# Performance work log

Hardware: AMD Instinct MI355X
Metric: run time of the kernel (lower is better)

Reference implementation:

```python
import jax, jax.numpy as jnp
import numpy as np

K = 20
EPS = 1e-6


def _vnt_linear(x, W):
    # VNT linear: rows normalized to sum to 1 (translation-equivariant channel mix)
    Wn = W / W.sum(axis=1, keepdims=True)
    return jnp.einsum('oi,bi...->bo...', Wn, x)


def _vn_lrelu(p, d):
    # Vector-neuron LeakyReLU with negative_slope=0: project p off -d half-space
    dot = jnp.sum(p * d, axis=2, keepdims=True)   # axis 2 is the 3-vector axis
    dns = jnp.sum(d * d, axis=2, keepdims=True)
    return jnp.where(dot >= 0, p, p - (dot / (dns + EPS)) * d)


def _vnt_lin_lrelu(x, W, D):
    p = _vnt_linear(x, W)
    d = jnp.einsum('oi,bi...->bo...', D, x)
    return _vn_lrelu(p, d)


def _graph_feature_cross(pts, k):
    # pts: [B, N, 3] -> edge features [B, 3(ch), 3(vec), N, k]
    B = pts.shape[0]
    xx = jnp.sum(pts * pts, axis=-1)                       # [B, N]
    inner = jnp.einsum('bnd,bmd->bnm', pts, pts)           # [B, N, N]
    pairwise = 2.0 * inner - xx[:, :, None] - xx[:, None, :]  # -||xi-xj||^2
    _, idx = jax.lax.top_k(pairwise, k)                    # [B, N, k]
    b_idx = jnp.arange(B)[:, None, None]
    nbrs = pts[b_idx, idx]                                 # [B, N, k, 3]
    ctr = jnp.broadcast_to(pts[:, :, None, :], nbrs.shape)
    cross = jnp.cross(nbrs, ctr)
    feat = jnp.stack([nbrs - ctr, ctr, cross], axis=3)     # [B, N, k, 3ch, 3vec]
    return jnp.transpose(feat, (0, 3, 4, 1, 2))            # [B, 3, 3, N, k]


def setup_inputs() -> dict:
    key = jax.random.key(0)
    ks = jax.random.split(key, 9)
    B, N, hidden = 8, 2048, 128

    def w(k_, o, i):  # positive weights -> stable row-sum normalization
        return jax.random.uniform(k_, (o, i), jnp.float32, 0.5 / i, 1.5 / i)

    def d(k_, o, i):
        return jax.random.normal(k_, (o, i), jnp.float32) / np.sqrt(i)

    return {
        'pc': jax.random.normal(ks[0], (B, N, 3), jnp.float32),
        'W_pos': w(ks[1], 64, 3), 'D_pos': d(ks[2], 64, 3),
        'W1': w(ks[3], hidden, 64), 'D1': d(ks[4], hidden, 64),
        'W2': w(ks[5], hidden, 2 * hidden), 'D2': d(ks[6], hidden, 2 * hidden),
        'W3': w(ks[7], hidden, 2 * hidden), 'D3': d(ks[8], hidden, 2 * hidden),
    }


def reference(pc, W_pos, D_pos, W1, D1, W2, D2, W3, D3):
    feat = _graph_feature_cross(pc, K)               # [B, 3, 3, N, k]
    net = _vnt_lin_lrelu(feat, W_pos, D_pos)         # [B, 64, 3, N, k]
    net = net.mean(axis=-1)                          # pool over k -> [B, 64, 3, N]
    net = _vnt_lin_lrelu(net, W1, D1)                # [B, 128, 3, N]
    pooled = jnp.broadcast_to(net.mean(axis=-1, keepdims=True), net.shape)
    net = jnp.concatenate([net, pooled], axis=1)     # [B, 256, 3, N]
    net = _vnt_lin_lrelu(net, W2, D2)                # [B, 128, 3, N]
    pooled = jnp.broadcast_to(net.mean(axis=-1, keepdims=True), net.shape)
    net = jnp.concatenate([net, pooled], axis=1)     # [B, 256, 3, N]
    net = _vnt_lin_lrelu(net, W3, D3)                # [B, 128, 3, N]
    c = net.mean(axis=-1)                            # pool over N -> [B, 128, 3]
    return c.reshape(pc.shape[0], -1)                # [B, 384]
```

## Files before the change

kernel.cpp:

```cpp
#include <hip/hip_runtime.h>
#include <hip/hip_bf16.h>
#include <math.h>

constexpr int B = 8;
constexpr int N = 2048;
constexpr int KNN = 20;
constexpr int H = 128;
constexpr int P = 3 * N;
constexpr int QPW = 8;

constexpr int OWT2   = 8448;
constexpr int OWT3   = 41216;
constexpr int OPS1   = 73984;
constexpr int OPS2   = 98560;
constexpr int OOUTS  = 123136;
constexpr int OWB1   = 160000;
constexpr int OWB2   = 176384;
constexpr int OWB3   = 209152;
constexpr int OXP0   = 569600;
constexpr int OXP2   = 569600;
constexpr int OXP1   = 6861056;

constexpr int ZERO_BASE = OPS1;
constexpr int ZERO_CNT  = 73728;

typedef __attribute__((ext_vector_type(8))) short bf16x8;
typedef __attribute__((ext_vector_type(4))) float f32x4;

__device__ __forceinline__ unsigned short f2bf(float x) {
  __hip_bfloat16 h = __float2bfloat16(x);
  return *(unsigned short*)&h;
}
__device__ __forceinline__ float bf2f(unsigned short u) {
  __hip_bfloat16 h;
  *(unsigned short*)&h = u;
  return __bfloat162float(h);
}
__device__ __forceinline__ unsigned int packhl(float x) {
  unsigned short hi = f2bf(x);
  float lo = x - bf2f(hi);
  unsigned short ls = f2bf(lo);
  return (unsigned)hi | ((unsigned)ls << 16);
}

__device__ __forceinline__ void wave_sort_key(unsigned long long& k, int lane) {
#pragma unroll
  for (int kk = 2; kk <= 64; kk <<= 1) {
#pragma unroll
    for (int j = kk >> 1; j > 0; j >>= 1) {
      unsigned long long pk =
          (unsigned long long)__shfl_xor((long long)k, j);
      bool iam_lower   = (lane & j) == 0;
      bool dir_desc    = (lane & kk) == 0;
      bool p_better    = pk > k;
      bool want_better = (dir_desc == iam_lower);
      k = (p_better == want_better) ? pk : k;
    }
  }
}

__global__ __launch_bounds__(512, 8) void knn_edge_kernel(
    const float* __restrict__ pc, const float* __restrict__ Wpos,
    const float* __restrict__ Dp,
    const float* __restrict__ W1, const float* __restrict__ D1,
    const float* __restrict__ W2, const float* __restrict__ D2,
    const float* __restrict__ W3, const float* __restrict__ D3,
    float* __restrict__ ws) {
  __shared__ float4 spt[N];
  __shared__ __align__(16) unsigned char sphase[QPW][640];
  int tid = threadIdx.x;
  int b = blockIdx.y;
  int bid = blockIdx.y * gridDim.x + blockIdx.x;
  int wv = tid >> 6, lane = tid & 63;
  unsigned short* Xp0 = (unsigned short*)(ws + OXP0);
  unsigned short* sbufw = (unsigned short*)sphase[wv];
  float4* erw = (float4*)sphase[wv];

  int o = lane;
  float w0 = Wpos[o * 3 + 0], w1 = Wpos[o * 3 + 1], w2 = Wpos[o * 3 + 2];
  float e0 = Dp[o * 3 + 0], e1 = Dp[o * 3 + 1], e2 = Dp[o * 3 + 2];

  {
    int zi = bid * 512 + tid;
    if (zi < ZERO_CNT) ws[ZERO_BASE + zi] = 0.f;
  }
  if (bid < 96) {
    int rr = bid * 8 + wv;
    const float* src;
    float* tdst = nullptr;
    unsigned int* pdst;
    int C, Cpack;
    bool norm;
    if (rr < 128)      { src = W1 + rr * 64;            C = 64;  Cpack = 64;  norm = true;
                         pdst = (unsigned int*)(ws + OWB1) + rr * 16; }
    else if (rr < 256) { int m = rr - 128; src = D1 + m * 64;  C = 64;  Cpack = 64;  norm = false;
                         pdst = (unsigned int*)(ws + OWB1) + (m + 128) * 16; }
    else if (rr < 384) { int m = rr - 256; src = W2 + m * 256; C = 256; Cpack = 128; norm = true;
                         pdst = (unsigned int*)(ws + OWB2) + m * 16; tdst = ws + OWT2 + m; }
    else if (rr < 512) { int m = rr - 384; src = D2 + m * 256; C = 256; Cpack = 128; norm = false;
                         pdst = (unsigned int*)(ws + OWB2) + (m + 128) * 16; tdst = ws + OWT2 + 128 + m; }
    else if (rr < 640) { int m = rr - 512; src = W3 + m * 256; C = 256; Cpack = 128; norm = true;
                         pdst = (unsigned int*)(ws + OWB3) + m * 16; tdst = ws + OWT3 + m; }
    else               { int m = rr - 640; src = D3 + m * 256; C = 256; Cpack = 128; norm = false;
                         pdst = (unsigned int*)(ws + OWB3) + (m + 128) * 16; tdst = ws + OWT3 + 128 + m; }
    float s = 1.f;
    if (norm) {
      float a = 0.f;
      for (int i = lane; i < C; i += 64) a += src[i];
#pragma unroll
      for (int off = 32; off > 0; off >>= 1) a += __shfl_xor(a, off);
      s = a;
    }
    for (int i = lane; i < C; i += 64) {
      float val = src[i] / s;
      if (i < Cpack) pdst[(i >> 4) * 4096 + (i & 15)] = packhl(val);
      if (tdst && i >= 128) tdst[(i - 128) * 256] = val;
    }
  }

  const float* pcb = pc + (size_t)b * N * 3;
  for (int i = tid; i < N; i += 512) {
    float x = pcb[i * 3 + 0], y = pcb[i * 3 + 1], z = pcb[i * 3 + 2];
    float xx = __fadd_rn(__fadd_rn(__fmul_rn(x, x), __fmul_rn(y, y)), __fmul_rn(z, z));
    spt[i] = make_float4(2.f * x, 2.f * y, 2.f * z, xx);
  }
  __syncthreads();
  int q = blockIdx.x * QPW + wv;
  float4 qp = spt[q];
  float qx = 0.5f * qp.x, qy = 0.5f * qp.y, qz = 0.5f * qp.z, qxx = qp.w;

  float dv[32];
  float lmax = -INFINITY;
#pragma unroll
  for (int i = 0; i < 32; ++i) {
    float4 m = spt[i * 64 + lane];
    float A = __fadd_rn(__fadd_rn(__fmul_rn(m.x, qx), __fmul_rn(m.y, qy)),
                        __fmul_rn(m.z, qz));
    float d = __fsub_rn(__fsub_rn(A, qxx), m.w);
    dv[i] = d;
    lmax = fmaxf(lmax, d);
  }

  float sv = lmax;
#pragma unroll
  for (int k = 2; k <= 64; k <<= 1) {
#pragma unroll
    for (int j = k >> 1; j > 0; j >>= 1) {
      float pv = __shfl_xor(sv, j);
      bool keep_max = ((lane & k) == 0) == ((lane & j) == 0);
      sv = keep_max ? fmaxf(sv, pv) : fminf(sv, pv);
    }
  }
  float tval = __shfl(sv, 19);

  unsigned msk = 0u;
#pragma unroll
  for (int i = 0; i < 32; ++i) msk |= (dv[i] >= tval) ? (1u << i) : 0u;
  int cnt = __popc(msk);
  int scan = cnt;
#pragma unroll
  for (int off = 1; off < 64; off <<= 1) {
    int t = __shfl_up(scan, off);
    scan += (lane >= off) ? t : 0;
  }
  int S = __shfl(scan, 63);
  int pos = scan - cnt;
  unsigned mm = msk;
  while (mm) {
    int i = __ffs(mm) - 1;
    mm &= mm - 1;
    if (pos < 192) sbufw[pos] = (unsigned short)(i * 64 + lane);
    ++pos;
  }

  auto distOf = [&](int m) -> float {
    float4 mp = spt[m];
    float A = __fadd_rn(__fadd_rn(__fmul_rn(mp.x, qx), __fmul_rn(mp.y, qy)),
                        __fmul_rn(mp.z, qz));
    return __fsub_rn(__fsub_rn(A, qxx), mp.w);
  };
  auto mkkey = [&](int m) -> unsigned long long {
    float d = distOf(m);
    unsigned u = __float_as_uint(d);
    u ^= (u >> 31) ? 0xFFFFFFFFu : 0x80000000u;
    return ((unsigned long long)u << 32) | (unsigned)(~m);
  };

  unsigned long long key = 0ULL;
  if (S <= 64) {
    if (lane < S) key = mkkey(sbufw[lane]);
    wave_sort_key(key, lane);
  } else if (S <= 192) {
    int p2 = 0;
    while (p2 < S) {
      if (lane >= KNN) {
        int t = p2 + lane - KNN;
        key = (t < S) ? mkkey(sbufw[t]) : 0ULL;
      }
      wave_sort_key(key, lane);
      p2 += 64 - KNN;
    }
  } else {
    int p2 = 0;
    while (p2 < N) {
      if (lane >= KNN) {
        int t = p2 + lane - KNN;
        key = (t < N) ? mkkey(t) : 0ULL;
      }
      wave_sort_key(key, lane);
      p2 += 64 - KNN;
    }
  }
  int cm = ~((unsigned)key);

  if (lane < KNN) {
    float4 t = spt[cm];
    float nx = 0.5f * t.x, ny = 0.5f * t.y, nz = 0.5f * t.z;
    float ex = nx - qx, ey = ny - qy, ez = nz - qz;
    float rx = ny * qz - nz * qy;
    float ry = nz * qx - nx * qz;
    float rz = nx * qy - ny * qx;
    erw[2 * lane + 0] = make_float4(ex, ey, ez, 0.f);
    erw[2 * lane + 1] = make_float4(rx, ry, rz, 0.f);
  }

  {
    float s = (w0 + w2) + w1;
    w0 = w0 / s; w1 = w1 / s; w2 = w2 / s;
  }
  float cx = qx, cy = qy, cz = qz;
  float pcx = w1 * cx, pcy = w1 * cy, pcz = w1 * cz;
  float dcx = e1 * cx, dcy = e1 * cy, dcz = e1 * cz;
  float ax = 0.f, ay = 0.f, az = 0.f;
#pragma unroll 4
  for (int k = 0; k < KNN; ++k) {
    float4 e4 = erw[2 * k + 0];
    float4 r4 = erw[2 * k + 1];
    float ex = e4.x, ey = e4.y, ez = e4.z;
    float rx = r4.x, ry = r4.y, rz = r4.z;
    float px = fmaf(w0, ex, fmaf(w2, rx, pcx));
    float py = fmaf(w0, ey, fmaf(w2, ry, pcy));
    float pz = fmaf(w0, ez, fmaf(w2, rz, pcz));
    float dx = fmaf(e0, ex, fmaf(e2, rx, dcx));
    float dy = fmaf(e0, ey, fmaf(e2, ry, dcy));
    float dz = fmaf(e0, ez, fmaf(e2, rz, dcz));
    float dot = fmaf(px, dx, fmaf(py, dy, pz * dz));
    float dns = fmaf(dx, dx, fmaf(dy, dy, dz * dz)) + 1e-6f;
    float r0 = __builtin_amdgcn_rcpf(dns);
    r0 = r0 * fmaf(-dns, r0, 2.0f);
    float f = (dot < 0.f) ? dot * r0 : 0.f;
    ax = fmaf(-f, dx, px) + ax;
    ay = fmaf(-f, dy, py) + ay;
    az = fmaf(-f, dz, pz) + az;
  }
  int pbase = ((q >> 4) * 48) + (q & 15);
  unsigned short* dst = Xp0 + ((size_t)b * P + pbase) * 128 + 2 * o;
  *(unsigned int*)(dst)              = packhl(ax * (1.f / 20.f));
  *(unsigned int*)(dst + 16 * 128)   = packhl(ay * (1.f / 20.f));
  *(unsigned int*)(dst + 32 * 128)   = packhl(az * (1.f / 20.f));
}

__global__ __launch_bounds__(256) void out_merge_kernel(
    const float* __restrict__ outs, float* __restrict__ out) {
  int idx = blockIdx.x * 256 + threadIdx.x;
  if (idx >= B * 384) return;
  float s = 0.f;
#pragma unroll
  for (int k = 0; k < 8; ++k) s += outs[k * 3072 + idx];
  out[idx] = s * (1.f / 2048.f);
}

template <int K2, bool HASPOOL, bool LAST>
__global__ __launch_bounds__(256, 4) void gemm_vnt_kernel(
    const unsigned short* __restrict__ Xp, const unsigned short* __restrict__ Wb,
    const float* __restrict__ ps, const float* __restrict__ Wt,
    unsigned short* __restrict__ Xq, float* __restrict__ pool,
    float* __restrict__ outs) {
  constexpr int KS = K2 / 32;
  constexpr int LDR = K2 + 8;
  constexpr int LDO = 132;
  __shared__ __align__(16) char smem[48 * LDO * 4];
  unsigned short* xt = (unsigned short*)smem;
  float* ot = (float*)smem;
  __shared__ float sb[768];
  __shared__ float spool[384];
  int tid = threadIdx.x;
  int bid = blockIdx.x;
  int b = bid >> 7;
  int nt = bid & 127;
  int p0 = nt * 48;

  int w = tid >> 6, lane = tid & 63;
  int q = lane >> 4, cl = lane & 15;

  for (int ch = tid; ch < 48 * (K2 / 8); ch += 256) {
    int rp = ch / (K2 / 8), cc = ch % (K2 / 8);
    *(uint4*)(xt + rp * LDR + cc * 8) =
        *(const uint4*)(Xp + ((size_t)b * P + p0 + rp) * K2 + cc * 8);
  }
  if (HASPOOL) {
    for (int i = tid; i < 384; i += 256) {
      float x = 0.f;
#pragma unroll
      for (int k = 0; k < 8; ++k) x += ps[k * 3072 + b * 384 + i];
      spool[i] = x * (1.f / 2048.f);
    }
  }

  bf16x8 acur[2][2], anxt[2][2];
#pragma unroll
  for (int t = 0; t < 2; ++t)
#pragma unroll
    for (int pd = 0; pd < 2; ++pd)
      acur[t][pd] = *(const bf16x8*)(Wb +
          (size_t)(32 * w + 16 * t + 128 * pd + cl) * 32 + q * 8);

  __syncthreads();
  if (HASPOOL) {
    float s0 = 0.f, s1 = 0.f, s2 = 0.f;
#pragma unroll 16
    for (int c = 0; c < 128; ++c) {
      float x = Wt[c * 256 + tid];
      s0 = fmaf(x, spool[c * 3 + 0], s0);
      s1 = fmaf(x, spool[c * 3 + 1], s1);
      s2 = fmaf(x, spool[c * 3 + 2], s2);
    }
    sb[tid * 3 + 0] = s0;
    sb[tid * 3 + 1] = s1;
    sb[tid * 3 + 2] = s2;
    __syncthreads();
  }

  f32x4 acc[2][2][3] = {};

#pragma unroll
  for (int ks = 0; ks < KS; ++ks) {
    if (ks + 1 < KS) {
#pragma unroll
      for (int t = 0; t < 2; ++t)
#pragma unroll
        for (int pd = 0; pd < 2; ++pd)
          anxt[t][pd] = *(const bf16x8*)(Wb +
              (size_t)(32 * w + 16 * t + 128 * pd + cl) * 32 + q * 8 +
              (ks + 1) * 8192);
    }
    bf16x8 bb[3];
#pragma unroll
    for (int v = 0; v < 3; ++v)
      bb[v] = *(const bf16x8*)(xt + (v * 16 + cl) * LDR + ks * 32 + q * 8);
#pragma unroll
    for (int t = 0; t < 2; ++t)
#pragma unroll
      for (int pd = 0; pd < 2; ++pd)
#pragma unroll
        for (int v = 0; v < 3; ++v)
          acc[t][pd][v] = __builtin_amdgcn_mfma_f32_16x16x32_bf16(
              acur[t][pd], bb[v], acc[t][pd][v], 0, 0, 0);
#pragma unroll
    for (int t = 0; t < 2; ++t)
#pragma unroll
      for (int pd = 0; pd < 2; ++pd)
        acur[t][pd] = anxt[t][pd];
  }
  __syncthreads();

#pragma unroll
  for (int t = 0; t < 2; ++t) {
    float res[3][4];
#pragma unroll
    for (int r = 0; r < 4; ++r) {
      int o = 32 * w + 16 * t + 4 * q + r;
      float pv[3], dvv[3];
#pragma unroll
      for (int v = 0; v < 3; ++v) {
        pv[v] = acc[t][0][v][r] + (HASPOOL ? sb[o * 3 + v] : 0.f);
        dvv[v] = acc[t][1][v][r] + (HASPOOL ? sb[(128 + o) * 3 + v] : 0.f);
      }
      float dot = fmaf(pv[0], dvv[0], fmaf(pv[1], dvv[1], pv[2] * dvv[2]));
      float dns = fmaf(dvv[0], dvv[0], fmaf(dvv[1], dvv[1], dvv[2] * dvv[2]));
      float f = (dot < 0.f) ? dot / (dns + 1e-6f) : 0.f;
#pragma unroll
      for (int v = 0; v < 3; ++v) res[v][r] = pv[v] - f * dvv[v];
    }
    int o0 = 32 * w + 16 * t + 4 * q;
#pragma unroll
    for (int v = 0; v < 3; ++v) {
      f32x4 rv = {res[v][0], res[v][1], res[v][2], res[v][3]};
      *(f32x4*)(ot + (v * 16 + cl) * LDO + o0) = rv;
    }
  }
  __syncthreads();

  int shadow = (nt & 7) * 3072;
  for (int s = tid; s < 384; s += 256) {
    int o = s / 3, v = s % 3;
    float a2 = 0.f;
#pragma unroll
    for (int c = 0; c < 16; ++c) a2 += ot[(v * 16 + c) * LDO + o];
    if (LAST) atomicAdd(outs + shadow + b * 384 + s, a2);
    else      atomicAdd(pool + shadow + b * 384 + s, a2);
  }

  if (!LAST) {
    for (int s = tid; s < 1536; s += 256) {
      int pix = s >> 5, c4 = s & 31;
      const float* src = ot + pix * LDO + c4 * 4;
      uint4 vv;
      vv.x = packhl(src[0]);
      vv.y = packhl(src[1]);
      vv.z = packhl(src[2]);
      vv.w = packhl(src[3]);
      *(uint4*)(Xq + ((size_t)b * P + p0 + pix) * 256 + c4 * 8) = vv;
    }
  }
}

extern "C" void kernel_launch(void* const* d_in, const int* in_sizes, int n_in,
                              void* d_out, int out_size, void* d_ws, size_t ws_size,
                              hipStream_t stream) {
  (void)in_sizes; (void)n_in; (void)out_size; (void)ws_size;
  const float* pc   = (const float*)d_in[0];
  const float* Wpos = (const float*)d_in[1];
  const float* Dpos = (const float*)d_in[2];
  const float* W1   = (const float*)d_in[3];
  const float* D1   = (const float*)d_in[4];
  const float* W2   = (const float*)d_in[5];
  const float* D2   = (const float*)d_in[6];
  const float* W3   = (const float*)d_in[7];
  const float* D3   = (const float*)d_in[8];
  float* out = (float*)d_out;
  float* ws  = (float*)d_ws;

  knn_edge_kernel<<<dim3(N / QPW, B), 512, 0, stream>>>(
      pc, Wpos, Dpos, W1, D1, W2, D2, W3, D3, ws);
  gemm_vnt_kernel<128, false, false><<<1024, 256, 0, stream>>>(
      (const unsigned short*)(ws + OXP0), (const unsigned short*)(ws + OWB1),
      nullptr, nullptr, (unsigned short*)(ws + OXP1), ws + OPS1, nullptr);
  gemm_vnt_kernel<256, true, false><<<1024, 256, 0, stream>>>(
      (const unsigned short*)(ws + OXP1), (const unsigned short*)(ws + OWB2),
      ws + OPS1, ws + OWT2, (unsigned short*)(ws + OXP2), ws + OPS2, nullptr);
  gemm_vnt_kernel<256, true, true><<<1024, 256, 0, stream>>>(
      (const unsigned short*)(ws + OXP2), (const unsigned short*)(ws + OWB3),
      ws + OPS2, ws + OWT3, nullptr, nullptr, ws + OOUTS);
  out_merge_kernel<<<12, 256, 0, stream>>>(ws + OOUTS, out);
}
```

Before: 167.8 us.

## Fuse first VNT GEMM layer into kNN edge kernel with in-block MFMA

```diff
diff --git a/kernel.cpp b/kernel.cpp
--- a/kernel.cpp
+++ b/kernel.cpp
@@ -7,22 +7,17 @@
 constexpr int KNN = 20;
 constexpr int H = 128;
 constexpr int P = 3 * N;
-constexpr int QPW = 8;
+constexpr int QPW = 16;
 
 constexpr int OWT2   = 8448;
 constexpr int OWT3   = 41216;
 constexpr int OPS1   = 73984;
 constexpr int OPS2   = 98560;
 constexpr int OOUTS  = 123136;
-constexpr int OWB1   = 160000;
 constexpr int OWB2   = 176384;
 constexpr int OWB3   = 209152;
-constexpr int OXP0   = 569600;
 constexpr int OXP2   = 569600;
 constexpr int OXP1   = 6861056;
-
-constexpr int ZERO_BASE = OPS1;
-constexpr int ZERO_CNT  = 73728;
 
 typedef __attribute__((ext_vector_type(8))) short bf16x8;
 typedef __attribute__((ext_vector_type(4))) float f32x4;
@@ -59,73 +54,75 @@
   }
 }
 
-__global__ __launch_bounds__(512, 8) void knn_edge_kernel(
+__global__ __launch_bounds__(1024, 8) void knn_edge_gemm1_kernel(
     const float* __restrict__ pc, const float* __restrict__ Wpos,
     const float* __restrict__ Dp,
     const float* __restrict__ W1, const float* __restrict__ D1,
     const float* __restrict__ W2, const float* __restrict__ D2,
     const float* __restrict__ W3, const float* __restrict__ D3,
     float* __restrict__ ws) {
-  __shared__ float4 spt[N];
+  __shared__ __align__(16) char spt_raw[32768];
   __shared__ __align__(16) unsigned char sphase[QPW][640];
+  float4* spt = (float4*)spt_raw;
+  unsigned short* xt = (unsigned short*)spt_raw;
+  unsigned int* xtu = (unsigned int*)spt_raw;
+  float* dt = (float*)spt_raw;
+
   int tid = threadIdx.x;
-  int b = blockIdx.y;
-  int bid = blockIdx.y * gridDim.x + blockIdx.x;
   int wv = tid >> 6, lane = tid & 63;
-  unsigned short* Xp0 = (unsigned short*)(ws + OXP0);
+  int cl = lane & 15, qq = lane >> 4;
+  int bx = blockIdx.x, b = blockIdx.y;
+  int bid = b * gridDim.x + bx;
   unsigned short* sbufw = (unsigned short*)sphase[wv];
   float4* erw = (float4*)sphase[wv];
+  unsigned short* Xq = (unsigned short*)(ws + OXP1);
+  float* pool = ws + OPS1;
 
   int o = lane;
   float w0 = Wpos[o * 3 + 0], w1 = Wpos[o * 3 + 1], w2 = Wpos[o * 3 + 2];
   float e0 = Dp[o * 3 + 0], e1 = Dp[o * 3 + 1], e2 = Dp[o * 3 + 2];
 
-  {
-    int zi = bid * 512 + tid;
-    if (zi < ZERO_CNT) ws[ZERO_BASE + zi] = 0.f;
-  }
-  if (bid < 96) {
-    int rr = bid * 8 + wv;
+  if (bid < 32) {
+    int rr = bid * 16 + wv;
     const float* src;
-    float* tdst = nullptr;
+    float* tdst;
     unsigned int* pdst;
-    int C, Cpack;
     bool norm;
-    if (rr < 128)      { src = W1 + rr * 64;            C = 64;  Cpack = 64;  norm = true;
-                         pdst = (unsigned int*)(ws + OWB1) + rr * 16; }
-    else if (rr < 256) { int m = rr - 128; src = D1 + m * 64;  C = 64;  Cpack = 64;  norm = false;
-                         pdst = (unsigned int*)(ws + OWB1) + (m + 128) * 16; }
-    else if (rr < 384) { int m = rr - 256; src = W2 + m * 256; C = 256; Cpack = 128; norm = true;
-                         pdst = (unsigned int*)(ws + OWB2) + m * 16; tdst = ws + OWT2 + m; }
-    else if (rr < 512) { int m = rr - 384; src = D2 + m * 256; C = 256; Cpack = 128; norm = false;
-                         pdst = (unsigned int*)(ws + OWB2) + (m + 128) * 16; tdst = ws + OWT2 + 128 + m; }
-    else if (rr < 640) { int m = rr - 512; src = W3 + m * 256; C = 256; Cpack = 128; norm = true;
-                         pdst = (unsigned int*)(ws + OWB3) + m * 16; tdst = ws + OWT3 + m; }
-    else               { int m = rr - 640; src = D3 + m * 256; C = 256; Cpack = 128; norm = false;
-                         pdst = (unsigned int*)(ws + OWB3) + (m + 128) * 16; tdst = ws + OWT3 + 128 + m; }
+    if (rr < 128)      { src = W2 + rr * 256; norm = true;
+                         pdst = (unsigned int*)(ws + OWB2) + rr * 16;
+                         tdst = ws + OWT2 + rr; }
+    else if (rr < 256) { int m = rr - 128; src = D2 + m * 256; norm = false;
+                         pdst = (unsigned int*)(ws + OWB2) + (m + 128) * 16;
+                         tdst = ws + OWT2 + 128 + m; }
+    else if (rr < 384) { int m = rr - 256; src = W3 + m * 256; norm = true;
+                         pdst = (unsigned int*)(ws + OWB3) + m * 16;
+                         tdst = ws + OWT3 + m; }
+    else               { int m = rr - 384; src = D3 + m * 256; norm = false;
+                         pdst = (unsigned int*)(ws + OWB3) + (m + 128) * 16;
+                         tdst = ws + OWT3 + 128 + m; }
     float s = 1.f;
     if (norm) {
       float a = 0.f;
-      for (int i = lane; i < C; i += 64) a += src[i];
+      for (int i = lane; i < 256; i += 64) a += src[i];
 #pragma unroll
       for (int off = 32; off > 0; off >>= 1) a += __shfl_xor(a, off);
       s = a;
     }
-    for (int i = lane; i < C; i += 64) {
+    for (int i = lane; i < 256; i += 64) {
       float val = src[i] / s;
-      if (i < Cpack) pdst[(i >> 4) * 4096 + (i & 15)] = packhl(val);
-      if (tdst && i >= 128) tdst[(i - 128) * 256] = val;
+      if (i < 128) pdst[(i >> 4) * 4096 + (i & 15)] = packhl(val);
+      else         tdst[(i - 128) * 256] = val;
     }
   }
 
   const float* pcb = pc + (size_t)b * N * 3;
-  for (int i = tid; i < N; i += 512) {
+  for (int i = tid; i < N; i += 1024) {
     float x = pcb[i * 3 + 0], y = pcb[i * 3 + 1], z = pcb[i * 3 + 2];
     float xx = __fadd_rn(__fadd_rn(__fmul_rn(x, x), __fmul_rn(y, y)), __fmul_rn(z, z));
     spt[i] = make_float4(2.f * x, 2.f * y, 2.f * z, xx);
   }
   __syncthreads();
-  int q = blockIdx.x * QPW + wv;
+  int q = bx * QPW + wv;
   float4 qp = spt[q];
   float qx = 0.5f * qp.x, qy = 0.5f * qp.y, qz = 0.5f * qp.z, qxx = qp.w;
 
@@ -253,11 +250,103 @@
     ay = fmaf(-f, dy, py) + ay;
     az = fmaf(-f, dz, pz) + az;
   }
-  int pbase = ((q >> 4) * 48) + (q & 15);
-  unsigned short* dst = Xp0 + ((size_t)b * P + pbase) * 128 + 2 * o;
-  *(unsigned int*)(dst)              = packhl(ax * (1.f / 20.f));
-  *(unsigned int*)(dst + 16 * 128)   = packhl(ay * (1.f / 20.f));
-  *(unsigned int*)(dst + 32 * 128)   = packhl(az * (1.f / 20.f));
+
+  int mrow = 16 * wv + cl;
+  const float* rowp = (wv < 8) ? (W1 + mrow * 64) : (D1 + (mrow - 128) * 64);
+  float4 cc[4];
+#pragma unroll
+  for (int ks = 0; ks < 4; ++ks)
+    cc[ks] = *(const float4*)(rowp + ks * 16 + qq * 4);
+  float sN = 1.f;
+  if (wv < 8) {
+    float p4 = 0.f;
+#pragma unroll
+    for (int ks = 0; ks < 4; ++ks)
+      p4 += (cc[ks].x + cc[ks].y) + (cc[ks].z + cc[ks].w);
+    p4 += __shfl_xor(p4, 16);
+    p4 += __shfl_xor(p4, 32);
+    sN = p4;
+  }
+  union AU { unsigned int u[4]; bf16x8 v8; } afr[4];
+#pragma unroll
+  for (int ks = 0; ks < 4; ++ks) {
+    const float* cf = (const float*)&cc[ks];
+#pragma unroll
+    for (int j = 0; j < 4; ++j) afr[ks].u[j] = packhl(cf[j] / sN);
+  }
+
+  __syncthreads();
+
+  xtu[(0 * 16 + wv) * 68 + lane] = packhl(ax * (1.f / 20.f));
+  xtu[(1 * 16 + wv) * 68 + lane] = packhl(ay * (1.f / 20.f));
+  xtu[(2 * 16 + wv) * 68 + lane] = packhl(az * (1.f / 20.f));
+  __syncthreads();
+
+  f32x4 acc[3] = {};
+#pragma unroll
+  for (int ks = 0; ks < 4; ++ks) {
+#pragma unroll
+    for (int v = 0; v < 3; ++v) {
+      bf16x8 bb = *(const bf16x8*)(xt + (v * 16 + cl) * 136 + ks * 32 + qq * 8);
+      acc[v] = __builtin_amdgcn_mfma_f32_16x16x32_bf16(afr[ks].v8, bb, acc[v], 0, 0, 0);
+    }
+  }
+  __syncthreads();
+
+  if (wv >= 8) {
+    int o0 = 16 * (wv - 8) + 4 * qq;
+#pragma unroll
+    for (int v = 0; v < 3; ++v)
+      *(f32x4*)(dt + (v * 16 + cl) * 132 + o0) = acc[v];
+  }
+  __syncthreads();
+
+  if (wv < 8) {
+    int o0 = 16 * wv + 4 * qq;
+    float res[3][4];
+#pragma unroll
+    for (int r = 0; r < 4; ++r) {
+      int oo = o0 + r;
+      float pv[3], dvv[3];
+#pragma unroll
+      for (int v = 0; v < 3; ++v) {
+        pv[v] = acc[v][r];
+        dvv[v] = dt[(v * 16 + cl) * 132 + oo];
+      }
+      float dot = fmaf(pv[0], dvv[0], fmaf(pv[1], dvv[1], pv[2] * dvv[2]));
+      float dns = fmaf(dvv[0], dvv[0], fmaf(dvv[1], dvv[1], dvv[2] * dvv[2]));
+      float f = (dot < 0.f) ? dot / (dns + 1e-6f) : 0.f;
+#pragma unroll
+      for (int v = 0; v < 3; ++v) res[v][r] = pv[v] - f * dvv[v];
+    }
+#pragma unroll
+    for (int v = 0; v < 3; ++v) {
+      f32x4 rv = {res[v][0], res[v][1], res[v][2], res[v][3]};
+      *(f32x4*)(dt + (v * 16 + cl) * 132 + o0) = rv;
+    }
+  }
+  __syncthreads();
+
+  int p0 = bx * 48;
+  for (int s = tid; s < 1536; s += 1024) {
+    int pix = s >> 5, c4 = s & 31;
+    const float* src = dt + pix * 132 + c4 * 4;
+    uint4 vv;
+    vv.x = packhl(src[0]);
+    vv.y = packhl(src[1]);
+    vv.z = packhl(src[2]);
+    vv.w = packhl(src[3]);
+    *(uint4*)(Xq + ((size_t)b * P + p0 + pix) * 256 + c4 * 8) = vv;
+  }
+
+  int shadow = (bx & 7) * 3072;
+  if (tid < 384) {
+    int oo = tid / 3, v = tid % 3;
+    float a2 = 0.f;
+#pragma unroll
+    for (int c = 0; c < 16; ++c) a2 += dt[(v * 16 + c) * 132 + oo];
+    atomicAdd(pool + shadow + b * 384 + tid, a2);
+  }
 }
 
 __global__ __launch_bounds__(256) void out_merge_kernel(
@@ -431,11 +520,9 @@
   float* out = (float*)d_out;
   float* ws  = (float*)d_ws;
 
-  knn_edge_kernel<<<dim3(N / QPW, B), 512, 0, stream>>>(
+  hipMemsetAsync(ws + OPS1, 0, 73728 * sizeof(float), stream);
+  knn_edge_gemm1_kernel<<<dim3(N / QPW, B), 1024, 0, stream>>>(
       pc, Wpos, Dpos, W1, D1, W2, D2, W3, D3, ws);
-  gemm_vnt_kernel<128, false, false><<<1024, 256, 0, stream>>>(
-      (const unsigned short*)(ws + OXP0), (const unsigned short*)(ws + OWB1),
-      nullptr, nullptr, (unsigned short*)(ws + OXP1), ws + OPS1, nullptr);
   gemm_vnt_kernel<256, true, false><<<1024, 256, 0, stream>>>(
       (const unsigned short*)(ws + OXP1), (const unsigned short*)(ws + OWB2),
       ws + OPS1, ws + OWT2, (unsigned short*)(ws + OXP2), ws + OPS2, nullptr);
```

Result: slower. 173.3 us (+3.3%).
